# Kernel tuning notes

Hardware: AMD Instinct MI355X
Metric: run time of the kernel (lower is better)

Reference implementation:

```python
import jax, jax.numpy as jnp
import numpy as np

B, Q, Fn, E, NL, L = 32, 16, 4096, 256, 8, 2


def _mapper(x, W, b):
    # stack of residual blocks: relu(x @ W + b) + x (dropout=0 at eval)
    for i in range(W.shape[0]):
        x = jax.nn.relu(x @ W[i] + b[i]) + x
    return x


def setup_inputs() -> dict:
    key = jax.random.key(0)
    ks = jax.random.split(key, 10)
    s = 1.0 / np.sqrt(E)
    return {
        "query": jax.random.normal(ks[0], (B, Q, E), jnp.float32),
        "features": jax.random.normal(ks[1], (B, Fn, E), jnp.float32),
        "values": jax.random.normal(ks[2], (B, Fn, E), jnp.float32),
        "attention_mask": jnp.ones((B, Fn), jnp.float32),
        "feature_time_weights": jax.random.uniform(ks[3], (B, Fn), jnp.float32),
        "Wq": jax.random.normal(ks[4], (L, E, E), jnp.float32) * s,
        "bq": jnp.zeros((L, E), jnp.float32),
        "Wf": jax.random.normal(ks[5], (L, E, E), jnp.float32) * s,
        "bf": jnp.zeros((L, E), jnp.float32),
        "Wv": jax.random.normal(ks[6], (L, E, E), jnp.float32) * s,
        "bv": jnp.zeros((L, E), jnp.float32),
        "Wc": jax.random.normal(ks[7], (L, E, E), jnp.float32) * s,
        "bc": jnp.zeros((L, E), jnp.float32),
        "Wout": jax.random.normal(ks[8], (E, NL), jnp.float32) * s,
        "bout": jnp.zeros((NL,), jnp.float32),
    }


def reference(query, features, values, attention_mask, feature_time_weights,
              Wq, bq, Wf, bf, Wv, bv, Wc, bc, Wout, bout):
    q = _mapper(query, Wq, bq)           # [B,Q,E]
    f = _mapper(features, Wf, bf)        # [B,F,E]
    # broadcast dot-product gate, done as batched matmul instead of repeat()
    attn = jax.nn.sigmoid(jnp.einsum('bqd,bfd->bqf', q, f))  # [B,Q,F]
    v = _mapper(values, Wv, bv)          # [B,F,E]
    w = attn * feature_time_weights[:, None, :] * attention_mask[:, None, :]
    pooled = jnp.einsum('bfe,bqf->bqe', v, w)  # weighted value pooling
    h = _mapper(pooled, Wc, bc)
    return h @ Wout + bout               # [B,Q,num_labels]
```

## Files before the change

kernel.cpp:

```cpp
#include <hip/hip_runtime.h>
#include <hip/hip_bf16.h>

#define B_   32
#define Q_   16
#define F_   4096
#define E_   256
#define NL_  8
#define FT   64
#define NTB  8
#define CH   8
#define TPB  512

typedef __attribute__((ext_vector_type(8))) __bf16 bf16x8_t;
typedef __attribute__((ext_vector_type(4))) __bf16 bf16x4_t;
typedef __attribute__((ext_vector_type(4))) float  f32x4;

__device__ __forceinline__ int swz(int r) {
  return ((r & 7) << 4) ^ (((r >> 3) & 3) << 5);
}
__device__ __forceinline__ int xoff(int r, int c2) {
  return r * 512 + (c2 ^ swz(r));
}
__device__ __forceinline__ unsigned short f2bf_bits(float f) {
  __bf16 h = (__bf16)f;
  return __builtin_bit_cast(unsigned short, h);
}

__global__ __launch_bounds__(256) void prep_kernel(
    const float* __restrict__ Wf, const float* __restrict__ Wv,
    const float* __restrict__ Wq, const float* __restrict__ Wc,
    unsigned short* __restrict__ WtF, unsigned short* __restrict__ WtV,
    unsigned short* __restrict__ WqT, unsigned short* __restrict__ WcT) {
  const int blk = blockIdx.x;
  const int t = threadIdx.x;
  __shared__ float ts[64][65];
  const int mat = blk >> 4;
  const int t16 = blk & 15;
  const int k0 = (t16 >> 2) * 64, n0 = (t16 & 3) * 64;
  const float* src;
  if (mat < 2) src = Wf + mat * 65536;
  else if (mat < 4) src = Wv + (mat - 2) * 65536;
  else if (mat < 6) src = Wq + (mat - 4) * 65536;
  else src = Wc + (mat - 6) * 65536;
#pragma unroll
  for (int p = 0; p < 16; ++p) {
    int e = p * 256 + t;
    int kk = e >> 6, nn = e & 63;
    ts[nn][kk] = src[(k0 + kk) * 256 + n0 + nn];
  }
  __syncthreads();
  unsigned short* dst;
  if (mat < 2) dst = WtF + mat * 65536;
  else if (mat < 4) dst = WtV + (mat - 2) * 65536;
  else if (mat < 6) dst = WqT + (mat - 4) * 65536;
  else dst = WcT + (mat - 6) * 65536;
#pragma unroll
  for (int p = 0; p < 16; ++p) {
    int e = p * 256 + t;
    int nn = e >> 6, kk = e & 63;
    dst[(n0 + nn) * 256 + k0 + kk] = f2bf_bits(ts[nn][kk]);
  }
}

struct StageRegs { f32x4 v[8]; };

__device__ __forceinline__ void stage_issue(StageRegs& s, const float* __restrict__ src, int tid) {
#pragma unroll
  for (int j = 0; j < 4; ++j) {
    int u = j * 512 + tid;
    int r = u >> 5;
    int c8 = (u & 31) << 3;
    const f32x4* p = (const f32x4*)(src + (size_t)r * E_ + c8);
    s.v[2 * j]     = __builtin_nontemporal_load(p);
    s.v[2 * j + 1] = __builtin_nontemporal_load(p + 1);
  }
}
__device__ __forceinline__ void stage_write(const StageRegs& s, char* Xs, int tid) {
#pragma unroll
  for (int j = 0; j < 4; ++j) {
    int u = j * 512 + tid;
    int r = u >> 5;
    int cb = (u & 31) << 4;
    f32x4 a = s.v[2 * j], b = s.v[2 * j + 1];
    bf16x8_t o;
    o[0] = (__bf16)a[0]; o[1] = (__bf16)a[1]; o[2] = (__bf16)a[2]; o[3] = (__bf16)a[3];
    o[4] = (__bf16)b[0]; o[5] = (__bf16)b[1]; o[6] = (__bf16)b[2]; o[7] = (__bf16)b[3];
    *(bf16x8_t*)(Xs + xoff(r, cb)) = o;
  }
}

struct WFrag { bf16x8_t w[8][2]; };

__device__ __forceinline__ void load_wfrag(WFrag& f, const unsigned short* __restrict__ Wt,
                                           int w, int lane) {
  const int c16 = lane & 15, kb = (lane >> 4) << 3;
  const unsigned short* r0 = Wt + (w * 32 + c16) * E_ + kb;
  const unsigned short* r1 = Wt + (w * 32 + 16 + c16) * E_ + kb;
#pragma unroll
  for (int ks = 0; ks < 8; ++ks) {
    f.w[ks][0] = *(const bf16x8_t*)(r0 + ks * 32);
    f.w[ks][1] = *(const bf16x8_t*)(r1 + ks * 32);
  }
}

__device__ __forceinline__ void layer_res(const char* __restrict__ Xin, char* __restrict__ Xout,
                                          const WFrag& wf, const float4 b0, const float4 b1,
                                          int w, int lane) {
  const int c16 = lane & 15, g = lane >> 4, kb = g << 3;
  f32x4 acc[2][4];
#pragma unroll
  for (int ef = 0; ef < 2; ++ef)
#pragma unroll
    for (int mf = 0; mf < 4; ++mf) acc[ef][mf] = (f32x4){0.f, 0.f, 0.f, 0.f};

#pragma unroll
  for (int ks = 0; ks < 8; ++ks) {
    const int k = ks * 32 + kb;
#pragma unroll
    for (int mf = 0; mf < 4; ++mf) {
      bf16x8_t xb = *(const bf16x8_t*)(Xin + xoff(mf * 16 + c16, k << 1));
      acc[0][mf] = __builtin_amdgcn_mfma_f32_16x16x32_bf16(wf.w[ks][0], xb, acc[0][mf], 0, 0, 0);
      acc[1][mf] = __builtin_amdgcn_mfma_f32_16x16x32_bf16(wf.w[ks][1], xb, acc[1][mf], 0, 0, 0);
    }
  }
#pragma unroll
  for (int ef = 0; ef < 2; ++ef) {
    const int e0 = w * 32 + ef * 16 + (g << 2);
    const float4 b4 = ef ? b1 : b0;
#pragma unroll
    for (int mf = 0; mf < 4; ++mf) {
      const int m = mf * 16 + c16;
      bf16x4_t old = *(const bf16x4_t*)(Xin + xoff(m, e0 << 1));
      bf16x4_t nw;
      nw[0] = (__bf16)(fmaxf(acc[ef][mf][0] + b4.x, 0.f) + (float)old[0]);
      nw[1] = (__bf16)(fmaxf(acc[ef][mf][1] + b4.y, 0.f) + (float)old[1]);
      nw[2] = (__bf16)(fmaxf(acc[ef][mf][2] + b4.z, 0.f) + (float)old[2]);
      nw[3] = (__bf16)(fmaxf(acc[ef][mf][3] + b4.w, 0.f) + (float)old[3]);
      *(bf16x4_t*)(Xout + xoff(m, e0 << 1)) = nw;
    }
  }
  __syncthreads();
}

__global__ __launch_bounds__(TPB) __attribute__((amdgpu_waves_per_eu(2, 2)))
void qmap_kernel(
    const float* __restrict__ query, const unsigned short* __restrict__ WqT,
    const float* __restrict__ bq, unsigned short* __restrict__ qmb) {
  const int blk = blockIdx.x;
  const int tid = threadIdx.x;
  const int lane = tid & 63, w = tid >> 6;
  const int g = lane >> 4;

  __shared__ __align__(128) char X[32768];
  __shared__ __align__(128) char Xt[32768];

  WFrag wf1, wf2;
  load_wfrag(wf1, WqT, w, lane);
  load_wfrag(wf2, WqT + 65536, w, lane);
  const float4 bA0 = *(const float4*)(bq + w * 32 + (g << 2));
  const float4 bA1 = *(const float4*)(bq + w * 32 + 16 + (g << 2));
  const float4 bB0 = *(const float4*)(bq + E_ + w * 32 + (g << 2));
  const float4 bB1 = *(const float4*)(bq + E_ + w * 32 + 16 + (g << 2));

  StageRegs s;
  stage_issue(s, query + (size_t)blk * 64 * E_, tid);
  stage_write(s, X, tid);
  __syncthreads();

  layer_res(X, Xt, wf1, bA0, bA1, w, lane);
  layer_res(Xt, X, wf2, bB0, bB1, w, lane);

#pragma unroll
  for (int j = 0; j < 4; ++j) {
    int u = j * 512 + tid;
    int r = u >> 5;
    bf16x8_t v = *(const bf16x8_t*)(X + xoff(r, (u & 31) << 4));
    *(bf16x8_t*)(qmb + (size_t)(blk * 64 + r) * E_ + ((u & 31) << 3)) = v;
  }
}

__global__ __launch_bounds__(TPB) __attribute__((amdgpu_waves_per_eu(2, 2)))
void passA_kernel(
    const float* __restrict__ features,
    const float* __restrict__ amask, const float* __restrict__ ftw,
    const unsigned short* __restrict__ WtF, const float* __restrict__ bfb,
    const unsigned short* __restrict__ qmb, unsigned short* __restrict__ Wsg) {
  const int bid0 = blockIdx.x;
  const int bid = (bid0 & 7) * 32 + (bid0 >> 3);
  const int b = bid >> 3, tb = bid & 7;
  const int tid = threadIdx.x;
  const int lane = tid & 63, w = tid >> 6;
  const int c16 = lane & 15, g = lane >> 4, kb = g << 3;

  __shared__ __align__(128) char X[2][32768];
  __shared__ __align__(128) char Xt[32768];

  WFrag wf1, wf2;
  load_wfrag(wf1, WtF, w, lane);
  load_wfrag(wf2, WtF + 65536, w, lane);
  const float4 bA0 = *(const float4*)(bfb + w * 32 + (g << 2));
  const float4 bA1 = *(const float4*)(bfb + w * 32 + 16 + (g << 2));
  const float4 bB0 = *(const float4*)(bfb + E_ + w * 32 + (g << 2));
  const float4 bB1 = *(const float4*)(bfb + E_ + w * 32 + 16 + (g << 2));

  const float* srcB = features + (size_t)(b * F_ + tb * CH * FT) * E_;

  StageRegs s;
  stage_issue(s, srcB, tid);
  stage_write(s, X[0], tid);
  __syncthreads();
  int cur = 0;

  for (int c = 0; c < CH; ++c) {
    if (c + 1 < CH) stage_issue(s, srcB + (size_t)(c + 1) * FT * E_, tid);

    layer_res(X[cur], Xt, wf1, bA0, bA1, w, lane);
    layer_res(Xt, X[cur], wf2, bB0, bB1, w, lane);

    if (c + 1 < CH) stage_write(s, X[cur ^ 1], tid);

    if (w < 4) {
      const int f0 = (tb * CH + c) * FT;
      f32x4 sv = (f32x4){0.f, 0.f, 0.f, 0.f};
      const int fl = w * 16 + c16;
      const unsigned short* qbase = qmb + (size_t)(b * Q_ + c16) * E_ + kb;
#pragma unroll
      for (int ks = 0; ks < 8; ++ks) {
        bf16x8_t qa = *(const bf16x8_t*)(qbase + ks * 32);
        bf16x8_t xb = *(const bf16x8_t*)(X[cur] + xoff(fl, (ks * 32 + kb) << 1));
        sv = __builtin_amdgcn_mfma_f32_16x16x32_bf16(qa, xb, sv, 0, 0, 0);
      }
      const int fg = f0 + fl;
      const float lw = ftw[b * F_ + fg] * amask[b * F_ + fg];
#pragma unroll
      for (int r = 0; r < 4; ++r) {
        float sg = 1.f / (1.f + __expf(-sv[r]));
        Wsg[((size_t)(b * Q_ + g * 4 + r)) * F_ + fg] = f2bf_bits(sg * lw);
      }
    }
    __syncthreads();
    cur ^= 1;
  }
}

__global__ __launch_bounds__(TPB) __attribute__((amdgpu_waves_per_eu(2, 2)))
void passB_kernel(
    const float* __restrict__ values,
    const unsigned short* __restrict__ WtV, const float* __restrict__ bvb,
    const unsigned short* __restrict__ Wsg, float* __restrict__ partials) {
  const int bid0 = blockIdx.x;
  const int bid = (bid0 & 7) * 32 + (bid0 >> 3);
  const int b = bid >> 3, tb = bid & 7;
  const int tid = threadIdx.x;
  const int lane = tid & 63, w = tid >> 6;
  const int c16 = lane & 15, g = lane >> 4, kb = g << 3;

  __shared__ __align__(128) char X[2][32768];
  __shared__ __align__(128) char Xt[32768];
  __shared__ __align__(16) unsigned short Wl[Q_][FT + 8];

  WFrag wf1, wf2;
  load_wfrag(wf1, WtV, w, lane);
  load_wfrag(wf2, WtV + 65536, w, lane);
  const float4 bA0 = *(const float4*)(bvb + w * 32 + (g << 2));
  const float4 bA1 = *(const float4*)(bvb + w * 32 + 16 + (g << 2));
  const float4 bB0 = *(const float4*)(bvb + E_ + w * 32 + (g << 2));
  const float4 bB1 = *(const float4*)(bvb + E_ + w * 32 + 16 + (g << 2));

  const float* srcB = values + (size_t)(b * F_ + tb * CH * FT) * E_;

  f32x4 pacc[2];
  pacc[0] = (f32x4){0.f, 0.f, 0.f, 0.f};
  pacc[1] = (f32x4){0.f, 0.f, 0.f, 0.f};

  StageRegs s;
  stage_issue(s, srcB, tid);
  stage_write(s, X[0], tid);
  __syncthreads();
  int cur = 0;

  for (int c = 0; c < CH; ++c) {
    const int f0 = (tb * CH + c) * FT;
    if (c + 1 < CH) stage_issue(s, srcB + (size_t)(c + 1) * FT * E_, tid);

    layer_res(X[cur], Xt, wf1, bA0, bA1, w, lane);

#pragma unroll
    for (int kk = 0; kk < 2; ++kk) {
      int idx = tid + kk * 512;
      int q = idx >> 6, j = idx & 63;
      Wl[q][j] = Wsg[((size_t)(b * Q_ + q)) * F_ + f0 + j];
    }

    layer_res(Xt, X[cur], wf2, bB0, bB1, w, lane);

    if (c + 1 < CH) stage_write(s, X[cur ^ 1], tid);

#pragma unroll
    for (int ks = 0; ks < FT / 32; ++ks) {
      bf16x8_t a = *(const bf16x8_t*)&Wl[c16][ks * 32 + kb];
#pragma unroll
      for (int nf = 0; nf < 2; ++nf) {
        const int e = w * 32 + nf * 16 + c16;
        bf16x8_t bb;
#pragma unroll
        for (int i = 0; i < 8; ++i) {
          const int f = ks * 32 + kb + i;
          bb[i] = *(const __bf16*)(X[cur] + xoff(f, e << 1));
        }
        pacc[nf] = __builtin_amdgcn_mfma_f32_16x16x32_bf16(a, bb, pacc[nf], 0, 0, 0);
      }
    }
    __syncthreads();
    cur ^= 1;
  }

#pragma unroll
  for (int nf = 0; nf < 2; ++nf) {
    const int e = w * 32 + nf * 16 + c16;
#pragma unroll
    for (int r = 0; r < 4; ++r) {
      const int q = g * 4 + r;
      partials[(((size_t)b * NTB + tb) * Q_ + q) * E_ + e] = pacc[nf][r];
    }
  }
}

__global__ __launch_bounds__(TPB) __attribute__((amdgpu_waves_per_eu(2, 2)))
void tail_kernel(
    const float* __restrict__ partials, const unsigned short* __restrict__ WcT,
    const float* __restrict__ bc, const float* __restrict__ Wout,
    const float* __restrict__ bout, float* __restrict__ out) {
  const int blk = blockIdx.x;
  const int tid = threadIdx.x;
  const int lane = tid & 63, w = tid >> 6;
  const int g = lane >> 4;

  __shared__ __align__(128) char X[32768];
  __shared__ __align__(128) char Xt[32768];

  WFrag wf1, wf2;
  load_wfrag(wf1, WcT, w, lane);
  load_wfrag(wf2, WcT + 65536, w, lane);
  const float4 bA0 = *(const float4*)(bc + w * 32 + (g << 2));
  const float4 bA1 = *(const float4*)(bc + w * 32 + 16 + (g << 2));
  const float4 bB0 = *(const float4*)(bc + E_ + w * 32 + (g << 2));
  const float4 bB1 = *(const float4*)(bc + E_ + w * 32 + 16 + (g << 2));

#pragma unroll
  for (int j = 0; j < 4; ++j) {
    int u = j * 512 + tid;
    int rl = u >> 5;
    int R = blk * 64 + rl;
    int b = R >> 4, q = R & 15;
    int e0 = (u & 31) << 3;
    f32x4 s0 = (f32x4){0.f, 0.f, 0.f, 0.f};
    f32x4 s1 = (f32x4){0.f, 0.f, 0.f, 0.f};
#pragma unroll
    for (int tb = 0; tb < NTB; ++tb) {
      const f32x4* p = (const f32x4*)(partials + (((size_t)(b * NTB + tb)) * Q_ + q) * E_ + e0);
      s0 += p[0];
      s1 += p[1];
    }
    bf16x8_t o;
    o[0] = (__bf16)s0[0]; o[1] = (__bf16)s0[1]; o[2] = (__bf16)s0[2]; o[3] = (__bf16)s0[3];
    o[4] = (__bf16)s1[0]; o[5] = (__bf16)s1[1]; o[6] = (__bf16)s1[2]; o[7] = (__bf16)s1[3];
    *(bf16x8_t*)(X + xoff(rl, e0 << 1)) = o;
  }
  __syncthreads();

  layer_res(X, Xt, wf1, bA0, bA1, w, lane);
  layer_res(Xt, X, wf2, bB0, bB1, w, lane);

  {
    const int rl = tid >> 3, n = tid & 7;
    const int R = blk * 64 + rl;
    float sum = bout[n];
#pragma unroll
    for (int k0 = 0; k0 < E_; k0 += 8) {
      bf16x8_t h8 = *(const bf16x8_t*)(X + xoff(rl, k0 << 1));
#pragma unroll
      for (int i = 0; i < 8; ++i)
        sum += (float)h8[i] * Wout[(k0 + i) * NL_ + n];
    }
    out[R * NL_ + n] = sum;
  }
}

extern "C" void kernel_launch(void* const* d_in, const int* in_sizes, int n_in,
                              void* d_out, int out_size, void* d_ws, size_t ws_size,
                              hipStream_t stream) {
  (void)in_sizes; (void)n_in; (void)out_size; (void)ws_size;
  const float* query    = (const float*)d_in[0];
  const float* features = (const float*)d_in[1];
  const float* values   = (const float*)d_in[2];
  const float* amask    = (const float*)d_in[3];
  const float* ftw      = (const float*)d_in[4];
  const float* Wq       = (const float*)d_in[5];
  const float* bq       = (const float*)d_in[6];
  const float* Wf       = (const float*)d_in[7];
  const float* bfb      = (const float*)d_in[8];
  const float* Wv       = (const float*)d_in[9];
  const float* bvb      = (const float*)d_in[10];
  const float* Wc       = (const float*)d_in[11];
  const float* bcb      = (const float*)d_in[12];
  const float* Wout     = (const float*)d_in[13];
  const float* bout     = (const float*)d_in[14];
  float* out = (float*)d_out;

  char* ws = (char*)d_ws;
  unsigned short* WtF = (unsigned short*)(ws);
  unsigned short* WtV = (unsigned short*)(ws + 262144);
  unsigned short* WqT = (unsigned short*)(ws + 524288);
  unsigned short* WcT = (unsigned short*)(ws + 786432);
  unsigned short* qmb = (unsigned short*)(ws + 1048576);
  unsigned short* Wsg = (unsigned short*)(ws + 1310720);
  float* partials     = (float*)(ws + 5505024);

  prep_kernel<<<128, 256, 0, stream>>>(Wf, Wv, Wq, Wc, WtF, WtV, WqT, WcT);
  qmap_kernel<<<(B_ * Q_) / 64, TPB, 0, stream>>>(query, WqT, bq, qmb);
  passA_kernel<<<B_ * NTB, TPB, 0, stream>>>(features, amask, ftw,
                                             WtF, bfb, qmb, Wsg);
  passB_kernel<<<B_ * NTB, TPB, 0, stream>>>(values, WtV, bvb, Wsg, partials);
  tail_kernel<<<(B_ * Q_) / 64, TPB, 0, stream>>>(partials, WcT, bcb, Wout, bout, out);
}
```

Before: 241.4 us.

## Double block size to 1024 threads and halve per-wave output columns

Blocks grow from 8 to 16 waves, and each wave now computes 16 output columns of every residual layer and of the pooling MFMA instead of 32. The weight fragments and accumulators held per wave shrink, and the waves-per-EU hint moves from 2 to 4. The aim is better latency hiding for the global staging loads and MFMA chains. In exchange each X fragment read from LDS feeds only one MFMA instead of two, so LDS traffic roughly doubles. Biases are also now read from global memory inside every layer call rather than once per kernel.

```diff
diff --git a/kernel.cpp b/kernel.cpp
--- a/kernel.cpp
+++ b/kernel.cpp
@@ -9,7 +9,7 @@
 #define FT   64
 #define NTB  8
 #define CH   8
-#define TPB  512
+#define TPB  1024
 
 typedef __attribute__((ext_vector_type(8))) __bf16 bf16x8_t;
 typedef __attribute__((ext_vector_type(4))) __bf16 bf16x4_t;
@@ -62,12 +62,12 @@
   }
 }
 
-struct StageRegs { f32x4 v[8]; };
+struct StageRegs { f32x4 v[4]; };
 
 __device__ __forceinline__ void stage_issue(StageRegs& s, const float* __restrict__ src, int tid) {
 #pragma unroll
-  for (int j = 0; j < 4; ++j) {
-    int u = j * 512 + tid;
+  for (int j = 0; j < 2; ++j) {
+    int u = j * 1024 + tid;
     int r = u >> 5;
     int c8 = (u & 31) << 3;
     const f32x4* p = (const f32x4*)(src + (size_t)r * E_ + c8);
@@ -77,8 +77,8 @@
 }
 __device__ __forceinline__ void stage_write(const StageRegs& s, char* Xs, int tid) {
 #pragma unroll
-  for (int j = 0; j < 4; ++j) {
-    int u = j * 512 + tid;
+  for (int j = 0; j < 2; ++j) {
+    int u = j * 1024 + tid;
     int r = u >> 5;
     int cb = (u & 31) << 4;
     f32x4 a = s.v[2 * j], b = s.v[2 * j + 1];
@@ -89,29 +89,23 @@
   }
 }
 
-struct WFrag { bf16x8_t w[8][2]; };
+struct WFrag { bf16x8_t w[8]; };
 
 __device__ __forceinline__ void load_wfrag(WFrag& f, const unsigned short* __restrict__ Wt,
                                            int w, int lane) {
   const int c16 = lane & 15, kb = (lane >> 4) << 3;
-  const unsigned short* r0 = Wt + (w * 32 + c16) * E_ + kb;
-  const unsigned short* r1 = Wt + (w * 32 + 16 + c16) * E_ + kb;
-#pragma unroll
-  for (int ks = 0; ks < 8; ++ks) {
-    f.w[ks][0] = *(const bf16x8_t*)(r0 + ks * 32);
-    f.w[ks][1] = *(const bf16x8_t*)(r1 + ks * 32);
-  }
+  const unsigned short* r0 = Wt + (w * 16 + c16) * E_ + kb;
+#pragma unroll
+  for (int ks = 0; ks < 8; ++ks) f.w[ks] = *(const bf16x8_t*)(r0 + ks * 32);
 }
 
 __device__ __forceinline__ void layer_res(const char* __restrict__ Xin, char* __restrict__ Xout,
-                                          const WFrag& wf, const float4 b0, const float4 b1,
+                                          const WFrag& wf, const float* __restrict__ bias_base,
                                           int w, int lane) {
   const int c16 = lane & 15, g = lane >> 4, kb = g << 3;
-  f32x4 acc[2][4];
-#pragma unroll
-  for (int ef = 0; ef < 2; ++ef)
-#pragma unroll
-    for (int mf = 0; mf < 4; ++mf) acc[ef][mf] = (f32x4){0.f, 0.f, 0.f, 0.f};
+  f32x4 acc[4];
+#pragma unroll
+  for (int mf = 0; mf < 4; ++mf) acc[mf] = (f32x4){0.f, 0.f, 0.f, 0.f};
 
 #pragma unroll
   for (int ks = 0; ks < 8; ++ks) {
@@ -119,37 +113,32 @@
 #pragma unroll
     for (int mf = 0; mf < 4; ++mf) {
       bf16x8_t xb = *(const bf16x8_t*)(Xin + xoff(mf * 16 + c16, k << 1));
-      acc[0][mf] = __builtin_amdgcn_mfma_f32_16x16x32_bf16(wf.w[ks][0], xb, acc[0][mf], 0, 0, 0);
-      acc[1][mf] = __builtin_amdgcn_mfma_f32_16x16x32_bf16(wf.w[ks][1], xb, acc[1][mf], 0, 0, 0);
-    }
-  }
-#pragma unroll
-  for (int ef = 0; ef < 2; ++ef) {
-    const int e0 = w * 32 + ef * 16 + (g << 2);
-    const float4 b4 = ef ? b1 : b0;
-#pragma unroll
-    for (int mf = 0; mf < 4; ++mf) {
-      const int m = mf * 16 + c16;
-      bf16x4_t old = *(const bf16x4_t*)(Xin + xoff(m, e0 << 1));
-      bf16x4_t nw;
-      nw[0] = (__bf16)(fmaxf(acc[ef][mf][0] + b4.x, 0.f) + (float)old[0]);
-      nw[1] = (__bf16)(fmaxf(acc[ef][mf][1] + b4.y, 0.f) + (float)old[1]);
-      nw[2] = (__bf16)(fmaxf(acc[ef][mf][2] + b4.z, 0.f) + (float)old[2]);
-      nw[3] = (__bf16)(fmaxf(acc[ef][mf][3] + b4.w, 0.f) + (float)old[3]);
-      *(bf16x4_t*)(Xout + xoff(m, e0 << 1)) = nw;
-    }
-  }
-  __syncthreads();
-}
-
-__global__ __launch_bounds__(TPB) __attribute__((amdgpu_waves_per_eu(2, 2)))
+      acc[mf] = __builtin_amdgcn_mfma_f32_16x16x32_bf16(wf.w[ks], xb, acc[mf], 0, 0, 0);
+    }
+  }
+  const int e0 = w * 16 + (g << 2);
+  const float4 b4 = *(const float4*)(bias_base + e0);
+#pragma unroll
+  for (int mf = 0; mf < 4; ++mf) {
+    const int m = mf * 16 + c16;
+    bf16x4_t old = *(const bf16x4_t*)(Xin + xoff(m, e0 << 1));
+    bf16x4_t nw;
+    nw[0] = (__bf16)(fmaxf(acc[mf][0] + b4.x, 0.f) + (float)old[0]);
+    nw[1] = (__bf16)(fmaxf(acc[mf][1] + b4.y, 0.f) + (float)old[1]);
+    nw[2] = (__bf16)(fmaxf(acc[mf][2] + b4.z, 0.f) + (float)old[2]);
+    nw[3] = (__bf16)(fmaxf(acc[mf][3] + b4.w, 0.f) + (float)old[3]);
+    *(bf16x4_t*)(Xout + xoff(m, e0 << 1)) = nw;
+  }
+  __syncthreads();
+}
+
+__global__ __launch_bounds__(TPB) __attribute__((amdgpu_waves_per_eu(4, 4)))
 void qmap_kernel(
     const float* __restrict__ query, const unsigned short* __restrict__ WqT,
     const float* __restrict__ bq, unsigned short* __restrict__ qmb) {
   const int blk = blockIdx.x;
   const int tid = threadIdx.x;
   const int lane = tid & 63, w = tid >> 6;
-  const int g = lane >> 4;
 
   __shared__ __align__(128) char X[32768];
   __shared__ __align__(128) char Xt[32768];
@@ -157,29 +146,25 @@
   WFrag wf1, wf2;
   load_wfrag(wf1, WqT, w, lane);
   load_wfrag(wf2, WqT + 65536, w, lane);
-  const float4 bA0 = *(const float4*)(bq + w * 32 + (g << 2));
-  const float4 bA1 = *(const float4*)(bq + w * 32 + 16 + (g << 2));
-  const float4 bB0 = *(const float4*)(bq + E_ + w * 32 + (g << 2));
-  const float4 bB1 = *(const float4*)(bq + E_ + w * 32 + 16 + (g << 2));
 
   StageRegs s;
   stage_issue(s, query + (size_t)blk * 64 * E_, tid);
   stage_write(s, X, tid);
   __syncthreads();
 
-  layer_res(X, Xt, wf1, bA0, bA1, w, lane);
-  layer_res(Xt, X, wf2, bB0, bB1, w, lane);
-
-#pragma unroll
-  for (int j = 0; j < 4; ++j) {
-    int u = j * 512 + tid;
+  layer_res(X, Xt, wf1, bq, w, lane);
+  layer_res(Xt, X, wf2, bq + E_, w, lane);
+
+#pragma unroll
+  for (int j = 0; j < 2; ++j) {
+    int u = j * 1024 + tid;
     int r = u >> 5;
     bf16x8_t v = *(const bf16x8_t*)(X + xoff(r, (u & 31) << 4));
     *(bf16x8_t*)(qmb + (size_t)(blk * 64 + r) * E_ + ((u & 31) << 3)) = v;
   }
 }
 
-__global__ __launch_bounds__(TPB) __attribute__((amdgpu_waves_per_eu(2, 2)))
+__global__ __launch_bounds__(TPB) __attribute__((amdgpu_waves_per_eu(4, 4)))
 void passA_kernel(
     const float* __restrict__ features,
     const float* __restrict__ amask, const float* __restrict__ ftw,
@@ -198,10 +183,6 @@
   WFrag wf1, wf2;
   load_wfrag(wf1, WtF, w, lane);
   load_wfrag(wf2, WtF + 65536, w, lane);
-  const float4 bA0 = *(const float4*)(bfb + w * 32 + (g << 2));
-  const float4 bA1 = *(const float4*)(bfb + w * 32 + 16 + (g << 2));
-  const float4 bB0 = *(const float4*)(bfb + E_ + w * 32 + (g << 2));
-  const float4 bB1 = *(const float4*)(bfb + E_ + w * 32 + 16 + (g << 2));
 
   const float* srcB = features + (size_t)(b * F_ + tb * CH * FT) * E_;
 
@@ -214,8 +195,8 @@
   for (int c = 0; c < CH; ++c) {
     if (c + 1 < CH) stage_issue(s, srcB + (size_t)(c + 1) * FT * E_, tid);
 
-    layer_res(X[cur], Xt, wf1, bA0, bA1, w, lane);
-    layer_res(Xt, X[cur], wf2, bB0, bB1, w, lane);
+    layer_res(X[cur], Xt, wf1, bfb, w, lane);
+    layer_res(Xt, X[cur], wf2, bfb + E_, w, lane);
 
     if (c + 1 < CH) stage_write(s, X[cur ^ 1], tid);
 
@@ -243,7 +224,7 @@
   }
 }
 
-__global__ __launch_bounds__(TPB) __attribute__((amdgpu_waves_per_eu(2, 2)))
+__global__ __launch_bounds__(TPB) __attribute__((amdgpu_waves_per_eu(4, 4)))
 void passB_kernel(
     const float* __restrict__ values,
     const unsigned short* __restrict__ WtV, const float* __restrict__ bvb,
@@ -262,16 +243,10 @@
   WFrag wf1, wf2;
   load_wfrag(wf1, WtV, w, lane);
   load_wfrag(wf2, WtV + 65536, w, lane);
-  const float4 bA0 = *(const float4*)(bvb + w * 32 + (g << 2));
-  const float4 bA1 = *(const float4*)(bvb + w * 32 + 16 + (g << 2));
-  const float4 bB0 = *(const float4*)(bvb + E_ + w * 32 + (g << 2));
-  const float4 bB1 = *(const float4*)(bvb + E_ + w * 32 + 16 + (g << 2));
 
   const float* srcB = values + (size_t)(b * F_ + tb * CH * FT) * E_;
 
-  f32x4 pacc[2];
-  pacc[0] = (f32x4){0.f, 0.f, 0.f, 0.f};
-  pacc[1] = (f32x4){0.f, 0.f, 0.f, 0.f};
+  f32x4 pacc = (f32x4){0.f, 0.f, 0.f, 0.f};
 
   StageRegs s;
   stage_issue(s, srcB, tid);
@@ -283,50 +258,44 @@
     const int f0 = (tb * CH + c) * FT;
     if (c + 1 < CH) stage_issue(s, srcB + (size_t)(c + 1) * FT * E_, tid);
 
-    layer_res(X[cur], Xt, wf1, bA0, bA1, w, lane);
-
-#pragma unroll
-    for (int kk = 0; kk < 2; ++kk) {
-      int idx = tid + kk * 512;
-      int q = idx >> 6, j = idx & 63;
+    layer_res(X[cur], Xt, wf1, bvb, w, lane);
+
+    {
+      int q = tid >> 6, j = tid & 63;
       Wl[q][j] = Wsg[((size_t)(b * Q_ + q)) * F_ + f0 + j];
     }
 
-    layer_res(Xt, X[cur], wf2, bB0, bB1, w, lane);
+    layer_res(Xt, X[cur], wf2, bvb + E_, w, lane);
 
     if (c + 1 < CH) stage_write(s, X[cur ^ 1], tid);
 
 #pragma unroll
     for (int ks = 0; ks < FT / 32; ++ks) {
       bf16x8_t a = *(const bf16x8_t*)&Wl[c16][ks * 32 + kb];
-#pragma unroll
-      for (int nf = 0; nf < 2; ++nf) {
-        const int e = w * 32 + nf * 16 + c16;
-        bf16x8_t bb;
-#pragma unroll
-        for (int i = 0; i < 8; ++i) {
-          const int f = ks * 32 + kb + i;
-          bb[i] = *(const __bf16*)(X[cur] + xoff(f, e << 1));
-        }
-        pacc[nf] = __builtin_amdgcn_mfma_f32_16x16x32_bf16(a, bb, pacc[nf], 0, 0, 0);
+      const int e = w * 16 + c16;
+      bf16x8_t bb;
+#pragma unroll
+      for (int i = 0; i < 8; ++i) {
+        const int f = ks * 32 + kb + i;
+        bb[i] = *(const __bf16*)(X[cur] + xoff(f, e << 1));
       }
+      pacc = __builtin_amdgcn_mfma_f32_16x16x32_bf16(a, bb, pacc, 0, 0, 0);
     }
     __syncthreads();
     cur ^= 1;
   }
 
-#pragma unroll
-  for (int nf = 0; nf < 2; ++nf) {
-    const int e = w * 32 + nf * 16 + c16;
+  {
+    const int e = w * 16 + c16;
 #pragma unroll
     for (int r = 0; r < 4; ++r) {
       const int q = g * 4 + r;
-      partials[(((size_t)b * NTB + tb) * Q_ + q) * E_ + e] = pacc[nf][r];
-    }
-  }
-}
-
-__global__ __launch_bounds__(TPB) __attribute__((amdgpu_waves_per_eu(2, 2)))
+      partials[(((size_t)b * NTB + tb) * Q_ + q) * E_ + e] = pacc[r];
+    }
+  }
+}
+
+__global__ __launch_bounds__(TPB) __attribute__((amdgpu_waves_per_eu(4, 4)))
 void tail_kernel(
     const float* __restrict__ partials, const unsigned short* __restrict__ WcT,
     const float* __restrict__ bc, const float* __restrict__ Wout,
@@ -334,7 +303,6 @@
   const int blk = blockIdx.x;
   const int tid = threadIdx.x;
   const int lane = tid & 63, w = tid >> 6;
-  const int g = lane >> 4;
 
   __shared__ __align__(128) char X[32768];
   __shared__ __align__(128) char Xt[32768];
@@ -342,14 +310,10 @@
   WFrag wf1, wf2;
   load_wfrag(wf1, WcT, w, lane);
   load_wfrag(wf2, WcT + 65536, w, lane);
-  const float4 bA0 = *(const float4*)(bc + w * 32 + (g << 2));
-  const float4 bA1 = *(const float4*)(bc + w * 32 + 16 + (g << 2));
-  const float4 bB0 = *(const float4*)(bc + E_ + w * 32 + (g << 2));
-  const float4 bB1 = *(const float4*)(bc + E_ + w * 32 + 16 + (g << 2));
-
-#pragma unroll
-  for (int j = 0; j < 4; ++j) {
-    int u = j * 512 + tid;
+
+#pragma unroll
+  for (int j = 0; j < 2; ++j) {
+    int u = j * 1024 + tid;
     int rl = u >> 5;
     int R = blk * 64 + rl;
     int b = R >> 4, q = R & 15;
@@ -369,10 +333,10 @@
   }
   __syncthreads();
 
-  layer_res(X, Xt, wf1, bA0, bA1, w, lane);
-  layer_res(Xt, X, wf2, bB0, bB1, w, lane);
-
-  {
+  layer_res(X, Xt, wf1, bc, w, lane);
+  layer_res(Xt, X, wf2, bc + E_, w, lane);
+
+  if (tid < 512) {
     const int rl = tid >> 3, n = tid & 7;
     const int R = blk * 64 + rl;
     float sum = bout[n];
```

New measurement: 298.3 us. 1.24x slower.

## Reload weight fragments per layer, update tiles in place, double grid blocks

Applied to the files above, without the earlier changes.

Weight fragments are no longer held in registers for the whole kernel; each layer reloads them from global/L2 and the residual update writes back into the same LDS tile after a barrier, dropping the separate Xt buffer. The waves_per_eu(2,2) constraint is removed and the grid is doubled (NTB 16, CH 4) to raise occupancy and parallelism. The prefetch of the next tile now completes synchronously before compute instead of overlapping via held registers. The intent is to cut register and LDS pressure, at the cost of repeated weight loads, an extra barrier per layer, more partials to reduce, and loss of load/compute overlap.

```diff
diff --git a/kernel.cpp b/kernel.cpp
--- a/kernel.cpp
+++ b/kernel.cpp
@@ -7,8 +7,8 @@
 #define E_   256
 #define NL_  8
 #define FT   64
-#define NTB  8
-#define CH   8
+#define NTB  16
+#define CH   4
 #define TPB  512
 
 typedef __attribute__((ext_vector_type(8))) __bf16 bf16x8_t;
@@ -62,26 +62,23 @@
   }
 }
 
-struct StageRegs { f32x4 v[8]; };
-
-__device__ __forceinline__ void stage_issue(StageRegs& s, const float* __restrict__ src, int tid) {
+__device__ __forceinline__ void stage_tile(char* Xs, const float* __restrict__ src, int tid) {
+  f32x4 v[8];
 #pragma unroll
   for (int j = 0; j < 4; ++j) {
     int u = j * 512 + tid;
     int r = u >> 5;
     int c8 = (u & 31) << 3;
     const f32x4* p = (const f32x4*)(src + (size_t)r * E_ + c8);
-    s.v[2 * j]     = __builtin_nontemporal_load(p);
-    s.v[2 * j + 1] = __builtin_nontemporal_load(p + 1);
-  }
-}
-__device__ __forceinline__ void stage_write(const StageRegs& s, char* Xs, int tid) {
+    v[2 * j]     = __builtin_nontemporal_load(p);
+    v[2 * j + 1] = __builtin_nontemporal_load(p + 1);
+  }
 #pragma unroll
   for (int j = 0; j < 4; ++j) {
     int u = j * 512 + tid;
     int r = u >> 5;
     int cb = (u & 31) << 4;
-    f32x4 a = s.v[2 * j], b = s.v[2 * j + 1];
+    f32x4 a = v[2 * j], b = v[2 * j + 1];
     bf16x8_t o;
     o[0] = (__bf16)a[0]; o[1] = (__bf16)a[1]; o[2] = (__bf16)a[2]; o[3] = (__bf16)a[3];
     o[4] = (__bf16)b[0]; o[5] = (__bf16)b[1]; o[6] = (__bf16)b[2]; o[7] = (__bf16)b[3];
@@ -89,24 +86,21 @@
   }
 }
 
-struct WFrag { bf16x8_t w[8][2]; };
-
-__device__ __forceinline__ void load_wfrag(WFrag& f, const unsigned short* __restrict__ Wt,
-                                           int w, int lane) {
-  const int c16 = lane & 15, kb = (lane >> 4) << 3;
+__device__ __forceinline__ void layer_ip(char* __restrict__ X,
+                                         const unsigned short* __restrict__ Wt,
+                                         const float* __restrict__ bias, int w, int lane) {
+  const int c16 = lane & 15, g = lane >> 4, kb = g << 3;
   const unsigned short* r0 = Wt + (w * 32 + c16) * E_ + kb;
   const unsigned short* r1 = Wt + (w * 32 + 16 + c16) * E_ + kb;
+
+  bf16x8_t wa0[8], wa1[8];
 #pragma unroll
   for (int ks = 0; ks < 8; ++ks) {
-    f.w[ks][0] = *(const bf16x8_t*)(r0 + ks * 32);
-    f.w[ks][1] = *(const bf16x8_t*)(r1 + ks * 32);
-  }
-}
-
-__device__ __forceinline__ void layer_res(const char* __restrict__ Xin, char* __restrict__ Xout,
-                                          const WFrag& wf, const float4 b0, const float4 b1,
-                                          int w, int lane) {
-  const int c16 = lane & 15, g = lane >> 4, kb = g << 3;
+    wa0[ks] = *(const bf16x8_t*)(r0 + ks * 32);
+    wa1[ks] = *(const bf16x8_t*)(r1 + ks * 32);
+  }
+  __builtin_amdgcn_sched_barrier(0);
+
   f32x4 acc[2][4];
 #pragma unroll
   for (int ef = 0; ef < 2; ++ef)
@@ -118,57 +112,46 @@
     const int k = ks * 32 + kb;
 #pragma unroll
     for (int mf = 0; mf < 4; ++mf) {
-      bf16x8_t xb = *(const bf16x8_t*)(Xin + xoff(mf * 16 + c16, k << 1));
-      acc[0][mf] = __builtin_amdgcn_mfma_f32_16x16x32_bf16(wf.w[ks][0], xb, acc[0][mf], 0, 0, 0);
-      acc[1][mf] = __builtin_amdgcn_mfma_f32_16x16x32_bf16(wf.w[ks][1], xb, acc[1][mf], 0, 0, 0);
-    }
-  }
+      bf16x8_t xb = *(const bf16x8_t*)(X + xoff(mf * 16 + c16, k << 1));
+      acc[0][mf] = __builtin_amdgcn_mfma_f32_16x16x32_bf16(wa0[ks], xb, acc[0][mf], 0, 0, 0);
+      acc[1][mf] = __builtin_amdgcn_mfma_f32_16x16x32_bf16(wa1[ks], xb, acc[1][mf], 0, 0, 0);
+    }
+  }
+  __syncthreads();
 #pragma unroll
   for (int ef = 0; ef < 2; ++ef) {
     const int e0 = w * 32 + ef * 16 + (g << 2);
-    const float4 b4 = ef ? b1 : b0;
+    const float4 b4 = *(const float4*)(bias + e0);
 #pragma unroll
     for (int mf = 0; mf < 4; ++mf) {
       const int m = mf * 16 + c16;
-      bf16x4_t old = *(const bf16x4_t*)(Xin + xoff(m, e0 << 1));
+      bf16x4_t* p = (bf16x4_t*)(X + xoff(m, e0 << 1));
+      bf16x4_t old = *p;
       bf16x4_t nw;
       nw[0] = (__bf16)(fmaxf(acc[ef][mf][0] + b4.x, 0.f) + (float)old[0]);
       nw[1] = (__bf16)(fmaxf(acc[ef][mf][1] + b4.y, 0.f) + (float)old[1]);
       nw[2] = (__bf16)(fmaxf(acc[ef][mf][2] + b4.z, 0.f) + (float)old[2]);
       nw[3] = (__bf16)(fmaxf(acc[ef][mf][3] + b4.w, 0.f) + (float)old[3]);
-      *(bf16x4_t*)(Xout + xoff(m, e0 << 1)) = nw;
-    }
-  }
-  __syncthreads();
-}
-
-__global__ __launch_bounds__(TPB) __attribute__((amdgpu_waves_per_eu(2, 2)))
-void qmap_kernel(
+      *p = nw;
+    }
+  }
+  __syncthreads();
+}
+
+__global__ __launch_bounds__(TPB) void qmap_kernel(
     const float* __restrict__ query, const unsigned short* __restrict__ WqT,
     const float* __restrict__ bq, unsigned short* __restrict__ qmb) {
   const int blk = blockIdx.x;
   const int tid = threadIdx.x;
   const int lane = tid & 63, w = tid >> 6;
-  const int g = lane >> 4;
 
   __shared__ __align__(128) char X[32768];
-  __shared__ __align__(128) char Xt[32768];
-
-  WFrag wf1, wf2;
-  load_wfrag(wf1, WqT, w, lane);
-  load_wfrag(wf2, WqT + 65536, w, lane);
-  const float4 bA0 = *(const float4*)(bq + w * 32 + (g << 2));
-  const float4 bA1 = *(const float4*)(bq + w * 32 + 16 + (g << 2));
-  const float4 bB0 = *(const float4*)(bq + E_ + w * 32 + (g << 2));
-  const float4 bB1 = *(const float4*)(bq + E_ + w * 32 + 16 + (g << 2));
-
-  StageRegs s;
-  stage_issue(s, query + (size_t)blk * 64 * E_, tid);
-  stage_write(s, X, tid);
-  __syncthreads();
-
-  layer_res(X, Xt, wf1, bA0, bA1, w, lane);
-  layer_res(Xt, X, wf2, bB0, bB1, w, lane);
+
+  stage_tile(X, query + (size_t)blk * 64 * E_, tid);
+  __syncthreads();
+
+  layer_ip(X, WqT, bq, w, lane);
+  layer_ip(X, WqT + 65536, bq + E_, w, lane);
 
 #pragma unroll
   for (int j = 0; j < 4; ++j) {
@@ -179,45 +162,31 @@
   }
 }
 
-__global__ __launch_bounds__(TPB) __attribute__((amdgpu_waves_per_eu(2, 2)))
-void passA_kernel(
+__global__ __launch_bounds__(TPB) void passA_kernel(
     const float* __restrict__ features,
     const float* __restrict__ amask, const float* __restrict__ ftw,
     const unsigned short* __restrict__ WtF, const float* __restrict__ bfb,
     const unsigned short* __restrict__ qmb, unsigned short* __restrict__ Wsg) {
   const int bid0 = blockIdx.x;
-  const int bid = (bid0 & 7) * 32 + (bid0 >> 3);
-  const int b = bid >> 3, tb = bid & 7;
+  const int bid = (bid0 & 7) * 64 + (bid0 >> 3);
+  const int b = bid >> 4, tb = bid & 15;
   const int tid = threadIdx.x;
   const int lane = tid & 63, w = tid >> 6;
   const int c16 = lane & 15, g = lane >> 4, kb = g << 3;
 
   __shared__ __align__(128) char X[2][32768];
-  __shared__ __align__(128) char Xt[32768];
-
-  WFrag wf1, wf2;
-  load_wfrag(wf1, WtF, w, lane);
-  load_wfrag(wf2, WtF + 65536, w, lane);
-  const float4 bA0 = *(const float4*)(bfb + w * 32 + (g << 2));
-  const float4 bA1 = *(const float4*)(bfb + w * 32 + 16 + (g << 2));
-  const float4 bB0 = *(const float4*)(bfb + E_ + w * 32 + (g << 2));
-  const float4 bB1 = *(const float4*)(bfb + E_ + w * 32 + 16 + (g << 2));
 
   const float* srcB = features + (size_t)(b * F_ + tb * CH * FT) * E_;
 
-  StageRegs s;
-  stage_issue(s, srcB, tid);
-  stage_write(s, X[0], tid);
+  stage_tile(X[0], srcB, tid);
   __syncthreads();
   int cur = 0;
 
   for (int c = 0; c < CH; ++c) {
-    if (c + 1 < CH) stage_issue(s, srcB + (size_t)(c + 1) * FT * E_, tid);
-
-    layer_res(X[cur], Xt, wf1, bA0, bA1, w, lane);
-    layer_res(Xt, X[cur], wf2, bB0, bB1, w, lane);
-
-    if (c + 1 < CH) stage_write(s, X[cur ^ 1], tid);
+    if (c + 1 < CH) stage_tile(X[cur ^ 1], srcB + (size_t)(c + 1) * FT * E_, tid);
+
+    layer_ip(X[cur], WtF, bfb, w, lane);
+    layer_ip(X[cur], WtF + 65536, bfb + E_, w, lane);
 
     if (w < 4) {
       const int f0 = (tb * CH + c) * FT;
@@ -243,29 +212,19 @@
   }
 }
 
-__global__ __launch_bounds__(TPB) __attribute__((amdgpu_waves_per_eu(2, 2)))
-void passB_kernel(
+__global__ __launch_bounds__(TPB) void passB_kernel(
     const float* __restrict__ values,
     const unsigned short* __restrict__ WtV, const float* __restrict__ bvb,
     const unsigned short* __restrict__ Wsg, float* __restrict__ partials) {
   const int bid0 = blockIdx.x;
-  const int bid = (bid0 & 7) * 32 + (bid0 >> 3);
-  const int b = bid >> 3, tb = bid & 7;
+  const int bid = (bid0 & 7) * 64 + (bid0 >> 3);
+  const int b = bid >> 4, tb = bid & 15;
   const int tid = threadIdx.x;
   const int lane = tid & 63, w = tid >> 6;
   const int c16 = lane & 15, g = lane >> 4, kb = g << 3;
 
   __shared__ __align__(128) char X[2][32768];
-  __shared__ __align__(128) char Xt[32768];
   __shared__ __align__(16) unsigned short Wl[Q_][FT + 8];
-
-  WFrag wf1, wf2;
-  load_wfrag(wf1, WtV, w, lane);
-  load_wfrag(wf2, WtV + 65536, w, lane);
-  const float4 bA0 = *(const float4*)(bvb + w * 32 + (g << 2));
-  const float4 bA1 = *(const float4*)(bvb + w * 32 + 16 + (g << 2));
-  const float4 bB0 = *(const float4*)(bvb + E_ + w * 32 + (g << 2));
-  const float4 bB1 = *(const float4*)(bvb + E_ + w * 32 + 16 + (g << 2));
 
   const float* srcB = values + (size_t)(b * F_ + tb * CH * FT) * E_;
 
@@ -273,17 +232,15 @@
   pacc[0] = (f32x4){0.f, 0.f, 0.f, 0.f};
   pacc[1] = (f32x4){0.f, 0.f, 0.f, 0.f};
 
-  StageRegs s;
-  stage_issue(s, srcB, tid);
-  stage_write(s, X[0], tid);
+  stage_tile(X[0], srcB, tid);
   __syncthreads();
   int cur = 0;
 
   for (int c = 0; c < CH; ++c) {
     const int f0 = (tb * CH + c) * FT;
-    if (c + 1 < CH) stage_issue(s, srcB + (size_t)(c + 1) * FT * E_, tid);
-
-    layer_res(X[cur], Xt, wf1, bA0, bA1, w, lane);
+    if (c + 1 < CH) stage_tile(X[cur ^ 1], srcB + (size_t)(c + 1) * FT * E_, tid);
+
+    layer_ip(X[cur], WtV, bvb, w, lane);
 
 #pragma unroll
     for (int kk = 0; kk < 2; ++kk) {
@@ -292,9 +249,7 @@
       Wl[q][j] = Wsg[((size_t)(b * Q_ + q)) * F_ + f0 + j];
     }
 
-    layer_res(Xt, X[cur], wf2, bB0, bB1, w, lane);
-
-    if (c + 1 < CH) stage_write(s, X[cur ^ 1], tid);
+    layer_ip(X[cur], WtV + 65536, bvb + E_, w, lane);
 
 #pragma unroll
     for (int ks = 0; ks < FT / 32; ++ks) {
@@ -326,26 +281,15 @@
   }
 }
 
-__global__ __launch_bounds__(TPB) __attribute__((amdgpu_waves_per_eu(2, 2)))
-void tail_kernel(
+__global__ __launch_bounds__(TPB) void tail_kernel(
     const float* __restrict__ partials, const unsigned short* __restrict__ WcT,
     const float* __restrict__ bc, const float* __restrict__ Wout,
     const float* __restrict__ bout, float* __restrict__ out) {
   const int blk = blockIdx.x;
   const int tid = threadIdx.x;
   const int lane = tid & 63, w = tid >> 6;
-  const int g = lane >> 4;
 
   __shared__ __align__(128) char X[32768];
-  __shared__ __align__(128) char Xt[32768];
-
-  WFrag wf1, wf2;
-  load_wfrag(wf1, WcT, w, lane);
-  load_wfrag(wf2, WcT + 65536, w, lane);
-  const float4 bA0 = *(const float4*)(bc + w * 32 + (g << 2));
-  const float4 bA1 = *(const float4*)(bc + w * 32 + 16 + (g << 2));
-  const float4 bB0 = *(const float4*)(bc + E_ + w * 32 + (g << 2));
-  const float4 bB1 = *(const float4*)(bc + E_ + w * 32 + 16 + (g << 2));
 
 #pragma unroll
   for (int j = 0; j < 4; ++j) {
@@ -369,8 +313,8 @@
   }
   __syncthreads();
 
-  layer_res(X, Xt, wf1, bA0, bA1, w, lane);
-  layer_res(Xt, X, wf2, bB0, bB1, w, lane);
+  layer_ip(X, WcT, bc, w, lane);
+  layer_ip(X, WcT + 65536, bc + E_, w, lane);
 
   {
     const int rl = tid >> 3, n = tid & 7;
```

After: 232.0 us. 1.04x faster.
